# Performance work log

Hardware: AMD Instinct MI355X
Metric: run time of the kernel (lower is better)

The kernel has to match this reference:

```python
import jax, jax.numpy as jnp
import numpy as np

INP_SIZE = 3072
HID = 1024
OUT = 768
N_RES = 2  # same block (shared weights) applied twice, as in the torch code
EPS = 1e-5


def _layernorm(x, g, b):
    m = jnp.mean(x, axis=-1, keepdims=True)
    v = jnp.mean((x - m) ** 2, axis=-1, keepdims=True)
    return (x - m) / jnp.sqrt(v + EPS) * g + b


def setup_inputs() -> dict:
    key = jax.random.key(0)
    ks = jax.random.split(key, 8)
    bsz = 8192
    s = 0.02
    return {
        "inp": jax.random.normal(ks[0], (bsz, INP_SIZE), dtype=jnp.float32),
        "y": jax.random.normal(ks[1], (bsz, OUT), dtype=jnp.float32),
        "ln1_g": jnp.ones((INP_SIZE,), jnp.float32),
        "ln1_b": jnp.zeros((INP_SIZE,), jnp.float32),
        "W1": jax.random.normal(ks[2], (INP_SIZE, HID), dtype=jnp.float32) * s,
        "b1": jnp.zeros((HID,), jnp.float32),
        "Wa": jax.random.normal(ks[3], (HID, HID), dtype=jnp.float32) * s,
        "ba": jnp.zeros((HID,), jnp.float32),
        "Wb": jax.random.normal(ks[4], (HID, HID), dtype=jnp.float32) * s,
        "bb": jnp.zeros((HID,), jnp.float32),
        "W2": jax.random.normal(ks[5], (HID, OUT), dtype=jnp.float32) * s,
        "b2": jnp.zeros((OUT,), jnp.float32),
        "ln2_g": jnp.ones((OUT,), jnp.float32),
        "ln2_b": jnp.zeros((OUT,), jnp.float32),
    }


def reference(inp, y, ln1_g, ln1_b, W1, b1, Wa, ba, Wb, bb, W2, b2, ln2_g, ln2_b):
    bsz = inp.shape[0]
    # backbone (dropout in eval mode = identity)
    h = _layernorm(inp, ln1_g, ln1_b) @ W1 + b1  # [bsz, HID]
    for _ in range(N_RES):  # shared block weights, applied twice
        r = jax.nn.relu(jax.nn.relu(h @ Wa + ba) @ Wb + bb)
        h = h + r
    pred_y = _layernorm(h @ W2 + b2, ln2_g, ln2_b)  # [bsz, OUT]

    # batched contrastive cosine-sim loss (replaces per-sample python loop)
    pn = pred_y / jnp.linalg.norm(pred_y, axis=1, keepdims=True)
    yn = y / jnp.linalg.norm(y, axis=1, keepdims=True)
    S = pn @ yn.T  # [bsz, bsz] cosine similarities
    loss = -jnp.sum(pn * yn) + jnp.sum(jax.nn.logsumexp(S, axis=1))

    acc = jnp.mean((jnp.argmax(S, axis=1) == jnp.arange(bsz)).astype(jnp.float32))
    return pred_y, loss, acc
```

## Files before the change

### kernel.cpp

```cpp
#include <hip/hip_runtime.h>
#include <hip/hip_fp16.h>
#include <cstdint>
#include <math.h>

#define INP  3072
#define HID  1024
#define OUTD 768
#define BSZ  8192

typedef _Float16 f16;
typedef _Float16 f16x8 __attribute__((ext_vector_type(8)));
typedef float    f32x4 __attribute__((ext_vector_type(4)));

static constexpr float LOG2E = 1.44269504088896340736f;
static constexpr float LN2   = 0.69314718055994530942f;

static constexpr size_t OFF_XH   = 0;
static constexpr size_t OFF_PN   = 0;
static constexpr size_t OFF_YN   = OFF_PN   + (size_t)BSZ*OUTD*2;
static constexpr size_t OFF_PSUM = OFF_YN   + (size_t)BSZ*OUTD*2;
static constexpr size_t OFF_PMAX = OFF_PSUM + (size_t)BSZ*64*4;
static constexpr size_t OFF_HB   = OFF_XH   + (size_t)BSZ*INP*2;
static constexpr size_t OFF_TT   = OFF_HB   + (size_t)BSZ*HID*2;
static constexpr size_t OFF_H    = OFF_TT   + (size_t)BSZ*OUTD*4;
static constexpr size_t OFF_W1T  = OFF_H    + (size_t)BSZ*HID*4;
static constexpr size_t OFF_WAT  = OFF_W1T  + (size_t)INP*HID*2;
static constexpr size_t OFF_WBT  = OFF_WAT  + (size_t)HID*HID*2;
static constexpr size_t OFF_W2T  = OFF_WBT  + (size_t)HID*HID*2;
static constexpr size_t OFF_DIAG = OFF_W2T  + (size_t)HID*OUTD*2;
static constexpr size_t OFF_ACC  = OFF_DIAG + (size_t)BSZ*4;

#define GL2LDS(gp, lp) __builtin_amdgcn_global_load_lds( \
    (__attribute__((address_space(1))) void*)(uintptr_t)(gp), \
    (__attribute__((address_space(3))) void*)(unsigned)(uintptr_t)(lp), 16, 0, 0)

__device__ __forceinline__ float blk_sum256(float v, float* sm) {
  #pragma unroll
  for (int d = 1; d < 64; d <<= 1) v += __shfl_xor(v, d, 64);
  int tid = threadIdx.x;
  __syncthreads();
  if ((tid & 63) == 0) sm[tid >> 6] = v;
  __syncthreads();
  return sm[0] + sm[1] + sm[2] + sm[3];
}

__global__ __launch_bounds__(256) void ln1_kernel(const float* __restrict__ inp,
    const float* __restrict__ g, const float* __restrict__ b, f16* __restrict__ xh) {
  __shared__ float sm[4];
  const int row = blockIdx.x, tid = threadIdx.x;
  const float* x = inp + (size_t)row * INP;
  float v[12]; float s = 0.f;
  #pragma unroll
  for (int i = 0; i < 12; i++) { v[i] = x[tid + i*256]; s += v[i]; }
  const float mean = blk_sum256(s, sm) * (1.f/INP);
  float s2 = 0.f;
  #pragma unroll
  for (int i = 0; i < 12; i++) { float d = v[i]-mean; s2 += d*d; }
  const float rstd = rsqrtf(blk_sum256(s2, sm) * (1.f/INP) + 1e-5f);
  f16* o = xh + (size_t)row * INP;
  #pragma unroll
  for (int i = 0; i < 12; i++) {
    int c = tid + i*256;
    o[c] = (f16)((v[i]-mean)*rstd*g[c] + b[c]);
  }
}

__global__ __launch_bounds__(256) void transpose_cast(const float* __restrict__ W,
    f16* __restrict__ Wt, int K, int N) {
  __shared__ float t[32][33];
  const int n0 = blockIdx.x*32, k0 = blockIdx.y*32;
  const int tx = threadIdx.x & 31, ty = threadIdx.x >> 5;
  #pragma unroll
  for (int i = 0; i < 32; i += 8) t[ty+i][tx] = W[(size_t)(k0+ty+i)*N + n0+tx];
  __syncthreads();
  #pragma unroll
  for (int i = 0; i < 32; i += 8) Wt[(size_t)(n0+ty+i)*K + k0+tx] = (f16)t[tx][ty+i];
}

__global__ __launch_bounds__(256) void ln2_kernel(const float* __restrict__ pre,
    const float* __restrict__ g, const float* __restrict__ b,
    float* __restrict__ outY, f16* __restrict__ pn) {
  __shared__ float sm[4];
  const int row = blockIdx.x, tid = threadIdx.x;
  const float* x = pre + (size_t)row * OUTD;
  float v[3]; float s = 0.f;
  #pragma unroll
  for (int i = 0; i < 3; i++) { v[i] = x[tid + i*256]; s += v[i]; }
  const float mean = blk_sum256(s, sm) * (1.f/OUTD);
  float s2 = 0.f;
  #pragma unroll
  for (int i = 0; i < 3; i++) { float d = v[i]-mean; s2 += d*d; }
  const float rstd = rsqrtf(blk_sum256(s2, sm) * (1.f/OUTD) + 1e-5f);
  float z[3]; float n2 = 0.f;
  #pragma unroll
  for (int i = 0; i < 3; i++) { int c = tid + i*256; z[i] = (v[i]-mean)*rstd*g[c] + b[c]; n2 += z[i]*z[i]; }
  const float rn = rsqrtf(blk_sum256(n2, sm)) * LOG2E;
  float* oy = outY + (size_t)row * OUTD;
  f16*   op = pn   + (size_t)row * OUTD;
  #pragma unroll
  for (int i = 0; i < 3; i++) { int c = tid + i*256; oy[c] = z[i]; op[c] = (f16)(z[i]*rn); }
}

__global__ __launch_bounds__(256) void yn_kernel(const float* __restrict__ y, f16* __restrict__ yn) {
  __shared__ float sm[4];
  const int row = blockIdx.x, tid = threadIdx.x;
  const float* x = y + (size_t)row * OUTD;
  float v[3]; float n2 = 0.f;
  #pragma unroll
  for (int i = 0; i < 3; i++) { v[i] = x[tid + i*256]; n2 += v[i]*v[i]; }
  const float rn = rsqrtf(blk_sum256(n2, sm));
  f16* o = yn + (size_t)row * OUTD;
  #pragma unroll
  for (int i = 0; i < 3; i++) { int c = tid + i*256; o[c] = (f16)(v[i]*rn); }
}

#define EPI_H   0
#define EPI_T   1
#define EPI_RES 2
#define EPI_P   3
#define EPI_S   4

template<int EPI>
__global__ __launch_bounds__(256) void gemm_bt(
    const f16* __restrict__ A, const f16* __restrict__ B, int K, int N,
    const float* __restrict__ bias, float* __restrict__ Cf, f16* __restrict__ Ch,
    const float* __restrict__ Hin,
    float* __restrict__ partsum, float* __restrict__ partmax, float* __restrict__ diagv)
{
  __shared__ alignas(16) f16 lA[2][128*32];
  __shared__ alignas(16) f16 lB[2][128*32];
  const int tid  = threadIdx.x;
  const int wave = tid >> 6, lane = tid & 63;
  const int m0 = blockIdx.x * 128, n0 = blockIdx.y * 128;
  const int srow  = tid >> 2;
  const int skc   = tid & 3;
  const int skc_sw = skc ^ ((srow >> 1) & 3);
  const f16* gA = A + (size_t)(m0 + srow) * K + skc_sw*8;
  const f16* gB = B + (size_t)(n0 + srow) * K + skc_sw*8;
  const int wm = wave & 1, wn = wave >> 1;
  const int fm = lane & 15;
  const int g4 = lane >> 4;
  const int ks = (fm >> 1) & 3;
  const int ck = ((g4 ^ ks) * 8);

  f32x4 acc[4][4];
  #pragma unroll
  for (int i = 0; i < 4; i++)
    #pragma unroll
    for (int j = 0; j < 4; j++) acc[i][j] = (f32x4){0.f,0.f,0.f,0.f};

  const int iters = K >> 5;
  auto stage = [&](int buf, int k0) {
    f16* lAw = &lA[buf][wave*16*32];
    f16* lBw = &lB[buf][wave*16*32];
    GL2LDS(gA + k0,                lAw);
    GL2LDS(gA + (size_t)64*K + k0, lAw + 64*32);
    GL2LDS(gB + k0,                lBw);
    GL2LDS(gB + (size_t)64*K + k0, lBw + 64*32);
  };

  stage(0, 0);
  __syncthreads();
  for (int it = 0; it < iters; ++it) {
    const int cur = it & 1;
    if (it + 1 < iters) stage(cur ^ 1, (it + 1) << 5);
    f16x8 af[4], bf[4];
    #pragma unroll
    for (int i = 0; i < 4; i++) af[i] = *(const f16x8*)&lA[cur][(wm*64 + i*16 + fm)*32 + ck];
    #pragma unroll
    for (int j = 0; j < 4; j++) bf[j] = *(const f16x8*)&lB[cur][(wn*64 + j*16 + fm)*32 + ck];
    #pragma unroll
    for (int i = 0; i < 4; i++)
      #pragma unroll
      for (int j = 0; j < 4; j++)
        acc[i][j] = __builtin_amdgcn_mfma_f32_16x16x32_f16(af[i], bf[j], acc[i][j], 0, 0, 0);
    __syncthreads();
  }

  if constexpr (EPI != EPI_S) {
    const int colb = n0 + wn*64;
    const int rowb = m0 + wm*64;
    #pragma unroll
    for (int i = 0; i < 4; i++) {
      #pragma unroll
      for (int j = 0; j < 4; j++) {
        const int col = colb + j*16 + fm;
        const float bs = bias[col];
        #pragma unroll
        for (int r = 0; r < 4; r++) {
          const int row = rowb + i*16 + g4*4 + r;
          float v = acc[i][j][r] + bs;
          const size_t idx = (size_t)row * N + col;
          if constexpr (EPI == EPI_H)        { Cf[idx] = v; Ch[idx] = (f16)v; }
          else if constexpr (EPI == EPI_T)   { v = fmaxf(v, 0.f); Ch[idx] = (f16)v; }
          else if constexpr (EPI == EPI_RES) { v = fmaxf(v, 0.f); v += Hin[idx]; Cf[idx] = v; Ch[idx] = (f16)v; }
          else                               { Cf[idx] = v; }
        }
      }
    }
  } else {
    __shared__ float redS[2][128], redM[2][128];
    const int bn = blockIdx.y;
    if (m0 == n0) {
      #pragma unroll
      for (int i = 0; i < 4; i++)
        #pragma unroll
        for (int j = 0; j < 4; j++) {
          const int col = n0 + wn*64 + j*16 + fm;
          #pragma unroll
          for (int r = 0; r < 4; r++) {
            const int row = m0 + wm*64 + i*16 + g4*4 + r;
            if (row == col) diagv[row] = acc[i][j][r];
          }
        }
    }
    #pragma unroll
    for (int i = 0; i < 4; i++) {
      #pragma unroll
      for (int r = 0; r < 4; r++) {
        const float a0 = acc[i][0][r], a1 = acc[i][1][r];
        const float a2 = acc[i][2][r], a3 = acc[i][3][r];
        float s  = exp2f(a0) + exp2f(a1) + exp2f(a2) + exp2f(a3);
        float mx = fmaxf(fmaxf(a0, a1), fmaxf(a2, a3));
        #pragma unroll
        for (int d = 1; d < 16; d <<= 1) {
          s  += __shfl_xor(s, d, 64);
          mx  = fmaxf(mx, __shfl_xor(mx, d, 64));
        }
        if (fm == 0) { const int lrow = wm*64 + i*16 + g4*4 + r; redS[wn][lrow] = s; redM[wn][lrow] = mx; }
      }
    }
    __syncthreads();
    if (tid < 128) {
      const float sa = redS[0][tid] + redS[1][tid];
      const float ma = fmaxf(redM[0][tid], redM[1][tid]);
      const size_t p = (size_t)bn * BSZ + m0 + tid;
      partsum[p] = sa; partmax[p] = ma;
    }
  }
}

__global__ __launch_bounds__(256) void reduce_rows(const float* __restrict__ partsum,
    const float* __restrict__ partmax, const float* __restrict__ diagv,
    float* __restrict__ accum) {
  __shared__ float sm[4];
  const int row = blockIdx.x*256 + threadIdx.x;
  float s = 0.f, mx = -1e30f;
  for (int i = 0; i < 64; i++) {
    s  += partsum[(size_t)i*BSZ + row];
    mx  = fmaxf(mx, partmax[(size_t)i*BSZ + row]);
  }
  const float dgs  = diagv[row];
  const float corr = (dgs >= mx) ? 1.f : 0.f;
  const float lse  = logf(s);
  const float dg   = dgs * LN2;
  const float lse_s = blk_sum256(lse, sm);
  const float dg_s  = blk_sum256(dg, sm);
  const float c_s   = blk_sum256(corr, sm);
  if (threadIdx.x == 0) {
    atomicAdd(&accum[0], lse_s);
    atomicAdd(&accum[1], dg_s);
    atomicAdd(&accum[2], c_s);
  }
}

__global__ void finalize_kernel(const float* __restrict__ accum, float* __restrict__ out) {
  out[0] = accum[0] - accum[1];
  out[1] = accum[2] * (1.f / BSZ);
}

extern "C" void kernel_launch(void* const* d_in, const int* in_sizes, int n_in,
                              void* d_out, int out_size, void* d_ws, size_t ws_size,
                              hipStream_t stream) {
  const float* inp  = (const float*)d_in[0];
  const float* y    = (const float*)d_in[1];
  const float* ln1g = (const float*)d_in[2];
  const float* ln1b = (const float*)d_in[3];
  const float* W1   = (const float*)d_in[4];
  const float* b1   = (const float*)d_in[5];
  const float* Wa   = (const float*)d_in[6];
  const float* ba   = (const float*)d_in[7];
  const float* Wb   = (const float*)d_in[8];
  const float* bb   = (const float*)d_in[9];
  const float* W2   = (const float*)d_in[10];
  const float* b2   = (const float*)d_in[11];
  const float* ln2g = (const float*)d_in[12];
  const float* ln2b = (const float*)d_in[13];
  float* out = (float*)d_out;

  char* ws = (char*)d_ws;
  f16*   XH   = (f16*)  (ws + OFF_XH);
  f16*   PN   = (f16*)  (ws + OFF_PN);
  f16*   YN   = (f16*)  (ws + OFF_YN);
  float* PSUM = (float*)(ws + OFF_PSUM);
  float* PMAX = (float*)(ws + OFF_PMAX);
  f16*   HB   = (f16*)  (ws + OFF_HB);
  f16*   T    = (f16*)  (ws + OFF_TT);
  float* PRE2 = (float*)(ws + OFF_TT);
  float* H    = (float*)(ws + OFF_H);
  f16*   W1T  = (f16*)  (ws + OFF_W1T);
  f16*   WAT  = (f16*)  (ws + OFF_WAT);
  f16*   WBT  = (f16*)  (ws + OFF_WBT);
  f16*   W2T  = (f16*)  (ws + OFF_W2T);
  float* DIAG = (float*)(ws + OFF_DIAG);
  float* ACC  = (float*)(ws + OFF_ACC);

  transpose_cast<<<dim3(HID/32,  INP/32), 256, 0, stream>>>(W1, W1T, INP, HID);
  transpose_cast<<<dim3(HID/32,  HID/32), 256, 0, stream>>>(Wa, WAT, HID, HID);
  transpose_cast<<<dim3(HID/32,  HID/32), 256, 0, stream>>>(Wb, WBT, HID, HID);
  transpose_cast<<<dim3(OUTD/32, HID/32), 256, 0, stream>>>(W2, W2T, HID, OUTD);

  ln1_kernel<<<BSZ, 256, 0, stream>>>(inp, ln1g, ln1b, XH);

  gemm_bt<EPI_H><<<dim3(BSZ/128, HID/128), 256, 0, stream>>>(
      XH, W1T, INP, HID, b1, H, HB, nullptr, nullptr, nullptr, nullptr);

  for (int it = 0; it < 2; it++) {
    gemm_bt<EPI_T><<<dim3(BSZ/128, HID/128), 256, 0, stream>>>(
        HB, WAT, HID, HID, ba, nullptr, T, nullptr, nullptr, nullptr, nullptr);
    gemm_bt<EPI_RES><<<dim3(BSZ/128, HID/128), 256, 0, stream>>>(
        T, WBT, HID, HID, bb, H, HB, H, nullptr, nullptr, nullptr);
  }

  gemm_bt<EPI_P><<<dim3(BSZ/128, OUTD/128), 256, 0, stream>>>(
      HB, W2T, HID, OUTD, b2, PRE2, nullptr, nullptr, nullptr, nullptr, nullptr);

  ln2_kernel<<<BSZ, 256, 0, stream>>>(PRE2, ln2g, ln2b, out, PN);
  yn_kernel<<<BSZ, 256, 0, stream>>>(y, YN);

  hipMemsetAsync(ACC, 0, 4*sizeof(float), stream);

  gemm_bt<EPI_S><<<dim3(BSZ/128, BSZ/128), 256, 0, stream>>>(
      PN, YN, OUTD, BSZ, nullptr, nullptr, nullptr, nullptr, PSUM, PMAX, DIAG);

  reduce_rows<<<BSZ/256, 256, 0, stream>>>(PSUM, PMAX, DIAG, ACC);
  finalize_kernel<<<1, 1, 0, stream>>>(ACC, out + (size_t)BSZ*OUTD);
}
```

Before: 588.7 us.

## Quantize similarity GEMM to int8, drop fp32 residual stream, fuse small kernels

The 8192x8192 cosine-similarity GEMM now runs on int8 MFMA, with normalized vectors quantized at scale 384 and rescaled in the epilogue. This halves operand bytes and doubles MFMA throughput relative to fp16. The fp32 residual copy H is removed, so the residual is carried only in fp16, which cuts global writes and reads. Separately, the four weight transposes become one launch, ln2 and yn become one launch, finalize is folded into reduce_rows via a last-block atomic counter, and ln1 is vectorized. The trade-off is precision: int8 similarities and an fp16-only residual may shift the loss and accuracy enough to fail tolerance.

```diff
diff --git a/kernel.cpp b/kernel.cpp
--- a/kernel.cpp
+++ b/kernel.cpp
@@ -10,20 +10,24 @@
 
 typedef _Float16 f16;
 typedef _Float16 f16x8 __attribute__((ext_vector_type(8)));
+typedef _Float16 f16x4 __attribute__((ext_vector_type(4)));
 typedef float    f32x4 __attribute__((ext_vector_type(4)));
+typedef int      i32x4 __attribute__((ext_vector_type(4)));
+typedef signed char s8;
 
 static constexpr float LOG2E = 1.44269504088896340736f;
 static constexpr float LN2   = 0.69314718055994530942f;
+static constexpr float QS    = 384.0f;
+static constexpr float CSC   = LOG2E / (QS * QS);
 
 static constexpr size_t OFF_XH   = 0;
 static constexpr size_t OFF_PN   = 0;
-static constexpr size_t OFF_YN   = OFF_PN   + (size_t)BSZ*OUTD*2;
-static constexpr size_t OFF_PSUM = OFF_YN   + (size_t)BSZ*OUTD*2;
+static constexpr size_t OFF_YN   = OFF_PN   + (size_t)BSZ*OUTD;
+static constexpr size_t OFF_PSUM = OFF_YN   + (size_t)BSZ*OUTD;
 static constexpr size_t OFF_PMAX = OFF_PSUM + (size_t)BSZ*64*4;
 static constexpr size_t OFF_HB   = OFF_XH   + (size_t)BSZ*INP*2;
 static constexpr size_t OFF_TT   = OFF_HB   + (size_t)BSZ*HID*2;
-static constexpr size_t OFF_H    = OFF_TT   + (size_t)BSZ*OUTD*4;
-static constexpr size_t OFF_W1T  = OFF_H    + (size_t)BSZ*HID*4;
+static constexpr size_t OFF_W1T  = OFF_TT   + (size_t)BSZ*OUTD*4;
 static constexpr size_t OFF_WAT  = OFF_W1T  + (size_t)INP*HID*2;
 static constexpr size_t OFF_WBT  = OFF_WAT  + (size_t)HID*HID*2;
 static constexpr size_t OFF_W2T  = OFF_WBT  + (size_t)HID*HID*2;
@@ -44,31 +48,56 @@
   return sm[0] + sm[1] + sm[2] + sm[3];
 }
 
+__device__ __forceinline__ s8 q8(float v) {
+  int q = __float2int_rn(v * QS);
+  q = q > 127 ? 127 : (q < -127 ? -127 : q);
+  return (s8)q;
+}
+
 __global__ __launch_bounds__(256) void ln1_kernel(const float* __restrict__ inp,
     const float* __restrict__ g, const float* __restrict__ b, f16* __restrict__ xh) {
   __shared__ float sm[4];
   const int row = blockIdx.x, tid = threadIdx.x;
-  const float* x = inp + (size_t)row * INP;
-  float v[12]; float s = 0.f;
-  #pragma unroll
-  for (int i = 0; i < 12; i++) { v[i] = x[tid + i*256]; s += v[i]; }
+  const float4* x4 = (const float4*)(inp + (size_t)row * INP);
+  float4 v[3]; float s = 0.f;
+  #pragma unroll
+  for (int i = 0; i < 3; i++) { v[i] = x4[tid + i*256]; s += v[i].x+v[i].y+v[i].z+v[i].w; }
   const float mean = blk_sum256(s, sm) * (1.f/INP);
   float s2 = 0.f;
   #pragma unroll
-  for (int i = 0; i < 12; i++) { float d = v[i]-mean; s2 += d*d; }
+  for (int i = 0; i < 3; i++) {
+    float dx=v[i].x-mean, dy=v[i].y-mean, dz=v[i].z-mean, dw=v[i].w-mean;
+    s2 += dx*dx+dy*dy+dz*dz+dw*dw;
+  }
   const float rstd = rsqrtf(blk_sum256(s2, sm) * (1.f/INP) + 1e-5f);
-  f16* o = xh + (size_t)row * INP;
-  #pragma unroll
-  for (int i = 0; i < 12; i++) {
-    int c = tid + i*256;
-    o[c] = (f16)((v[i]-mean)*rstd*g[c] + b[c]);
-  }
-}
-
-__global__ __launch_bounds__(256) void transpose_cast(const float* __restrict__ W,
-    f16* __restrict__ Wt, int K, int N) {
+  const float4* g4p = (const float4*)g;
+  const float4* b4p = (const float4*)b;
+  f16x4* o4 = (f16x4*)(xh + (size_t)row * INP);
+  #pragma unroll
+  for (int i = 0; i < 3; i++) {
+    const int c = tid + i*256;
+    const float4 gg = g4p[c], bb = b4p[c];
+    f16x4 t;
+    t[0] = (f16)((v[i].x-mean)*rstd*gg.x + bb.x);
+    t[1] = (f16)((v[i].y-mean)*rstd*gg.y + bb.y);
+    t[2] = (f16)((v[i].z-mean)*rstd*gg.z + bb.z);
+    t[3] = (f16)((v[i].w-mean)*rstd*gg.w + bb.w);
+    o4[c] = t;
+  }
+}
+
+__global__ __launch_bounds__(256) void transpose_all(
+    const float* __restrict__ W1, const float* __restrict__ Wa,
+    const float* __restrict__ Wb, const float* __restrict__ W2,
+    f16* __restrict__ W1T, f16* __restrict__ WAT,
+    f16* __restrict__ WBT, f16* __restrict__ W2T) {
   __shared__ float t[32][33];
-  const int n0 = blockIdx.x*32, k0 = blockIdx.y*32;
+  const int bI = blockIdx.x;
+  const float* W; f16* Wt; int K, N, n0, k0;
+  if (bI < 3072)      { int tt = bI;      W = W1; Wt = W1T; K = INP; N = HID;  n0 = (tt & 31)*32; k0 = (tt >> 5)*32; }
+  else if (bI < 4096) { int tt = bI-3072; W = Wa; Wt = WAT; K = HID; N = HID;  n0 = (tt & 31)*32; k0 = (tt >> 5)*32; }
+  else if (bI < 5120) { int tt = bI-4096; W = Wb; Wt = WBT; K = HID; N = HID;  n0 = (tt & 31)*32; k0 = (tt >> 5)*32; }
+  else                { int tt = bI-5120; W = W2; Wt = W2T; K = HID; N = OUTD; int kq = tt/24; n0 = (tt - kq*24)*32; k0 = kq*32; }
   const int tx = threadIdx.x & 31, ty = threadIdx.x >> 5;
   #pragma unroll
   for (int i = 0; i < 32; i += 8) t[ty+i][tx] = W[(size_t)(k0+ty+i)*N + n0+tx];
@@ -77,55 +106,54 @@
   for (int i = 0; i < 32; i += 8) Wt[(size_t)(n0+ty+i)*K + k0+tx] = (f16)t[tx][ty+i];
 }
 
-__global__ __launch_bounds__(256) void ln2_kernel(const float* __restrict__ pre,
+__global__ __launch_bounds__(256) void ln2_yn(const float* __restrict__ pre,
     const float* __restrict__ g, const float* __restrict__ b,
-    float* __restrict__ outY, f16* __restrict__ pn) {
+    const float* __restrict__ y,
+    float* __restrict__ outY, s8* __restrict__ pn, s8* __restrict__ yn) {
   __shared__ float sm[4];
-  const int row = blockIdx.x, tid = threadIdx.x;
-  const float* x = pre + (size_t)row * OUTD;
-  float v[3]; float s = 0.f;
-  #pragma unroll
-  for (int i = 0; i < 3; i++) { v[i] = x[tid + i*256]; s += v[i]; }
-  const float mean = blk_sum256(s, sm) * (1.f/OUTD);
-  float s2 = 0.f;
-  #pragma unroll
-  for (int i = 0; i < 3; i++) { float d = v[i]-mean; s2 += d*d; }
-  const float rstd = rsqrtf(blk_sum256(s2, sm) * (1.f/OUTD) + 1e-5f);
-  float z[3]; float n2 = 0.f;
-  #pragma unroll
-  for (int i = 0; i < 3; i++) { int c = tid + i*256; z[i] = (v[i]-mean)*rstd*g[c] + b[c]; n2 += z[i]*z[i]; }
-  const float rn = rsqrtf(blk_sum256(n2, sm)) * LOG2E;
-  float* oy = outY + (size_t)row * OUTD;
-  f16*   op = pn   + (size_t)row * OUTD;
-  #pragma unroll
-  for (int i = 0; i < 3; i++) { int c = tid + i*256; oy[c] = z[i]; op[c] = (f16)(z[i]*rn); }
-}
-
-__global__ __launch_bounds__(256) void yn_kernel(const float* __restrict__ y, f16* __restrict__ yn) {
-  __shared__ float sm[4];
-  const int row = blockIdx.x, tid = threadIdx.x;
-  const float* x = y + (size_t)row * OUTD;
-  float v[3]; float n2 = 0.f;
-  #pragma unroll
-  for (int i = 0; i < 3; i++) { v[i] = x[tid + i*256]; n2 += v[i]*v[i]; }
-  const float rn = rsqrtf(blk_sum256(n2, sm));
-  f16* o = yn + (size_t)row * OUTD;
-  #pragma unroll
-  for (int i = 0; i < 3; i++) { int c = tid + i*256; o[c] = (f16)(v[i]*rn); }
+  const int tid = threadIdx.x;
+  if ((int)blockIdx.x < BSZ) {
+    const int row = blockIdx.x;
+    const float* x = pre + (size_t)row * OUTD;
+    float v[3]; float s = 0.f;
+    #pragma unroll
+    for (int i = 0; i < 3; i++) { v[i] = x[tid + i*256]; s += v[i]; }
+    const float mean = blk_sum256(s, sm) * (1.f/OUTD);
+    float s2 = 0.f;
+    #pragma unroll
+    for (int i = 0; i < 3; i++) { float d = v[i]-mean; s2 += d*d; }
+    const float rstd = rsqrtf(blk_sum256(s2, sm) * (1.f/OUTD) + 1e-5f);
+    float z[3]; float n2 = 0.f;
+    #pragma unroll
+    for (int i = 0; i < 3; i++) { int c = tid + i*256; z[i] = (v[i]-mean)*rstd*g[c] + b[c]; n2 += z[i]*z[i]; }
+    const float rn = rsqrtf(blk_sum256(n2, sm));
+    float* oy = outY + (size_t)row * OUTD;
+    s8*   op = pn   + (size_t)row * OUTD;
+    #pragma unroll
+    for (int i = 0; i < 3; i++) { int c = tid + i*256; oy[c] = z[i]; op[c] = q8(z[i]*rn); }
+  } else {
+    const int row = blockIdx.x - BSZ;
+    const float* x = y + (size_t)row * OUTD;
+    float v[3]; float n2 = 0.f;
+    #pragma unroll
+    for (int i = 0; i < 3; i++) { v[i] = x[tid + i*256]; n2 += v[i]*v[i]; }
+    const float rn = rsqrtf(blk_sum256(n2, sm));
+    s8* o = yn + (size_t)row * OUTD;
+    #pragma unroll
+    for (int i = 0; i < 3; i++) { int c = tid + i*256; o[c] = q8(v[i]*rn); }
+  }
 }
 
 #define EPI_H   0
 #define EPI_T   1
 #define EPI_RES 2
 #define EPI_P   3
-#define EPI_S   4
 
 template<int EPI>
 __global__ __launch_bounds__(256) void gemm_bt(
     const f16* __restrict__ A, const f16* __restrict__ B, int K, int N,
     const float* __restrict__ bias, float* __restrict__ Cf, f16* __restrict__ Ch,
-    const float* __restrict__ Hin,
-    float* __restrict__ partsum, float* __restrict__ partmax, float* __restrict__ diagv)
+    const f16* __restrict__ Hin)
 {
   __shared__ alignas(16) f16 lA[2][128*32];
   __shared__ alignas(16) f16 lB[2][128*32];
@@ -177,72 +205,127 @@
     __syncthreads();
   }
 
-  if constexpr (EPI != EPI_S) {
-    const int colb = n0 + wn*64;
-    const int rowb = m0 + wm*64;
-    #pragma unroll
-    for (int i = 0; i < 4; i++) {
+  const int colb = n0 + wn*64;
+  const int rowb = m0 + wm*64;
+  #pragma unroll
+  for (int i = 0; i < 4; i++) {
+    #pragma unroll
+    for (int j = 0; j < 4; j++) {
+      const int col = colb + j*16 + fm;
+      const float bs = bias[col];
+      #pragma unroll
+      for (int r = 0; r < 4; r++) {
+        const int row = rowb + i*16 + g4*4 + r;
+        float v = acc[i][j][r] + bs;
+        const size_t idx = (size_t)row * N + col;
+        if constexpr (EPI == EPI_H)        { Ch[idx] = (f16)v; }
+        else if constexpr (EPI == EPI_T)   { v = fmaxf(v, 0.f); Ch[idx] = (f16)v; }
+        else if constexpr (EPI == EPI_RES) { v = fmaxf(v, 0.f); v += (float)Hin[idx]; Ch[idx] = (f16)v; }
+        else                               { Cf[idx] = v; }
+      }
+    }
+  }
+}
+
+__global__ __launch_bounds__(256) void gemm_s8(
+    const s8* __restrict__ A, const s8* __restrict__ B,
+    float* __restrict__ partsum, float* __restrict__ partmax, float* __restrict__ diagv)
+{
+  __shared__ alignas(16) s8 lA[2][128*64];
+  __shared__ alignas(16) s8 lB[2][128*64];
+  __shared__ float redS[2][128], redM[2][128];
+  const int K = OUTD;
+  const int tid = threadIdx.x;
+  const int wave = tid >> 6, lane = tid & 63;
+  const int m0 = blockIdx.x * 128, n0 = blockIdx.y * 128;
+  const int srow = tid >> 2;
+  const int cl   = tid & 3;
+  const int cg   = cl ^ ((srow ^ (srow >> 2)) & 3);
+  const s8* gA = A + (size_t)(m0 + srow) * K + cg*16;
+  const s8* gB = B + (size_t)(n0 + srow) * K + cg*16;
+  const int wm = wave & 1, wn = wave >> 1;
+  const int fm = lane & 15;
+  const int g4 = lane >> 4;
+  const int ksw = (fm ^ (fm >> 2)) & 3;
+  const int ck8 = (g4 ^ ksw) * 16;
+
+  i32x4 acc[4][4];
+  #pragma unroll
+  for (int i = 0; i < 4; i++)
+    #pragma unroll
+    for (int j = 0; j < 4; j++) acc[i][j] = (i32x4){0,0,0,0};
+
+  auto stage = [&](int buf, int k0) {
+    s8* lAw = &lA[buf][wave*16*64];
+    s8* lBw = &lB[buf][wave*16*64];
+    GL2LDS(gA + k0,                lAw);
+    GL2LDS(gA + (size_t)64*K + k0, lAw + 64*64);
+    GL2LDS(gB + k0,                lBw);
+    GL2LDS(gB + (size_t)64*K + k0, lBw + 64*64);
+  };
+
+  stage(0, 0);
+  __syncthreads();
+  const int iters = K / 64;
+  for (int it = 0; it < iters; ++it) {
+    const int cur = it & 1;
+    if (it + 1 < iters) stage(cur ^ 1, (it + 1) * 64);
+    i32x4 af[4], bf[4];
+    #pragma unroll
+    for (int i = 0; i < 4; i++) af[i] = *(const i32x4*)&lA[cur][(wm*64 + i*16 + fm)*64 + ck8];
+    #pragma unroll
+    for (int j = 0; j < 4; j++) bf[j] = *(const i32x4*)&lB[cur][(wn*64 + j*16 + fm)*64 + ck8];
+    #pragma unroll
+    for (int i = 0; i < 4; i++)
+      #pragma unroll
+      for (int j = 0; j < 4; j++)
+        acc[i][j] = __builtin_amdgcn_mfma_i32_16x16x64_i8(af[i], bf[j], acc[i][j], 0, 0, 0);
+    __syncthreads();
+  }
+
+  if (m0 == n0) {
+    #pragma unroll
+    for (int i = 0; i < 4; i++)
       #pragma unroll
       for (int j = 0; j < 4; j++) {
-        const int col = colb + j*16 + fm;
-        const float bs = bias[col];
+        const int col = n0 + wn*64 + j*16 + fm;
         #pragma unroll
         for (int r = 0; r < 4; r++) {
-          const int row = rowb + i*16 + g4*4 + r;
-          float v = acc[i][j][r] + bs;
-          const size_t idx = (size_t)row * N + col;
-          if constexpr (EPI == EPI_H)        { Cf[idx] = v; Ch[idx] = (f16)v; }
-          else if constexpr (EPI == EPI_T)   { v = fmaxf(v, 0.f); Ch[idx] = (f16)v; }
-          else if constexpr (EPI == EPI_RES) { v = fmaxf(v, 0.f); v += Hin[idx]; Cf[idx] = v; Ch[idx] = (f16)v; }
-          else                               { Cf[idx] = v; }
+          const int row = m0 + wm*64 + i*16 + g4*4 + r;
+          if (row == col) diagv[row] = (float)acc[i][j][r] * CSC;
         }
       }
+  }
+  #pragma unroll
+  for (int i = 0; i < 4; i++) {
+    #pragma unroll
+    for (int r = 0; r < 4; r++) {
+      const float a0 = (float)acc[i][0][r] * CSC;
+      const float a1 = (float)acc[i][1][r] * CSC;
+      const float a2 = (float)acc[i][2][r] * CSC;
+      const float a3 = (float)acc[i][3][r] * CSC;
+      float s  = exp2f(a0) + exp2f(a1) + exp2f(a2) + exp2f(a3);
+      float mx = fmaxf(fmaxf(a0, a1), fmaxf(a2, a3));
+      #pragma unroll
+      for (int d = 1; d < 16; d <<= 1) {
+        s  += __shfl_xor(s, d, 64);
+        mx  = fmaxf(mx, __shfl_xor(mx, d, 64));
+      }
+      if (fm == 0) { const int lrow = wm*64 + i*16 + g4*4 + r; redS[wn][lrow] = s; redM[wn][lrow] = mx; }
     }
-  } else {
-    __shared__ float redS[2][128], redM[2][128];
-    const int bn = blockIdx.y;
-    if (m0 == n0) {
-      #pragma unroll
-      for (int i = 0; i < 4; i++)
-        #pragma unroll
-        for (int j = 0; j < 4; j++) {
-          const int col = n0 + wn*64 + j*16 + fm;
-          #pragma unroll
-          for (int r = 0; r < 4; r++) {
-            const int row = m0 + wm*64 + i*16 + g4*4 + r;
-            if (row == col) diagv[row] = acc[i][j][r];
-          }
-        }
-    }
-    #pragma unroll
-    for (int i = 0; i < 4; i++) {
-      #pragma unroll
-      for (int r = 0; r < 4; r++) {
-        const float a0 = acc[i][0][r], a1 = acc[i][1][r];
-        const float a2 = acc[i][2][r], a3 = acc[i][3][r];
-        float s  = exp2f(a0) + exp2f(a1) + exp2f(a2) + exp2f(a3);
-        float mx = fmaxf(fmaxf(a0, a1), fmaxf(a2, a3));
-        #pragma unroll
-        for (int d = 1; d < 16; d <<= 1) {
-          s  += __shfl_xor(s, d, 64);
-          mx  = fmaxf(mx, __shfl_xor(mx, d, 64));
-        }
-        if (fm == 0) { const int lrow = wm*64 + i*16 + g4*4 + r; redS[wn][lrow] = s; redM[wn][lrow] = mx; }
-      }
-    }
-    __syncthreads();
-    if (tid < 128) {
-      const float sa = redS[0][tid] + redS[1][tid];
-      const float ma = fmaxf(redM[0][tid], redM[1][tid]);
-      const size_t p = (size_t)bn * BSZ + m0 + tid;
-      partsum[p] = sa; partmax[p] = ma;
-    }
+  }
+  __syncthreads();
+  if (tid < 128) {
+    const float sa = redS[0][tid] + redS[1][tid];
+    const float ma = fmaxf(redM[0][tid], redM[1][tid]);
+    const size_t p = (size_t)blockIdx.y * BSZ + m0 + tid;
+    partsum[p] = sa; partmax[p] = ma;
   }
 }
 
 __global__ __launch_bounds__(256) void reduce_rows(const float* __restrict__ partsum,
     const float* __restrict__ partmax, const float* __restrict__ diagv,
-    float* __restrict__ accum) {
+    float* __restrict__ accum, float* __restrict__ out) {
   __shared__ float sm[4];
   const int row = blockIdx.x*256 + threadIdx.x;
   float s = 0.f, mx = -1e30f;
@@ -261,12 +344,16 @@
     atomicAdd(&accum[0], lse_s);
     atomicAdd(&accum[1], dg_s);
     atomicAdd(&accum[2], c_s);
-  }
-}
-
-__global__ void finalize_kernel(const float* __restrict__ accum, float* __restrict__ out) {
-  out[0] = accum[0] - accum[1];
-  out[1] = accum[2] * (1.f / BSZ);
+    __threadfence();
+    const unsigned old = atomicAdd((unsigned*)&accum[3], 1u);
+    if (old == gridDim.x - 1) {
+      const float a0 = atomicAdd(&accum[0], 0.f);
+      const float a1 = atomicAdd(&accum[1], 0.f);
+      const float a2 = atomicAdd(&accum[2], 0.f);
+      out[0] = a0 - a1;
+      out[1] = a2 * (1.f / BSZ);
+    }
+  }
 }
 
 extern "C" void kernel_launch(void* const* d_in, const int* in_sizes, int n_in,
@@ -290,14 +377,13 @@
 
   char* ws = (char*)d_ws;
   f16*   XH   = (f16*)  (ws + OFF_XH);
-  f16*   PN   = (f16*)  (ws + OFF_PN);
-  f16*   YN   = (f16*)  (ws + OFF_YN);
+  s8*    PN   = (s8*)   (ws + OFF_PN);
+  s8*    YN   = (s8*)   (ws + OFF_YN);
   float* PSUM = (float*)(ws + OFF_PSUM);
   float* PMAX = (float*)(ws + OFF_PMAX);
   f16*   HB   = (f16*)  (ws + OFF_HB);
   f16*   T    = (f16*)  (ws + OFF_TT);
   float* PRE2 = (float*)(ws + OFF_TT);
-  float* H    = (float*)(ws + OFF_H);
   f16*   W1T  = (f16*)  (ws + OFF_W1T);
   f16*   WAT  = (f16*)  (ws + OFF_WAT);
   f16*   WBT  = (f16*)  (ws + OFF_WBT);
@@ -305,34 +391,27 @@
   float* DIAG = (float*)(ws + OFF_DIAG);
   float* ACC  = (float*)(ws + OFF_ACC);
 
-  transpose_cast<<<dim3(HID/32,  INP/32), 256, 0, stream>>>(W1, W1T, INP, HID);
-  transpose_cast<<<dim3(HID/32,  HID/32), 256, 0, stream>>>(Wa, WAT, HID, HID);
-  transpose_cast<<<dim3(HID/32,  HID/32), 256, 0, stream>>>(Wb, WBT, HID, HID);
-  transpose_cast<<<dim3(OUTD/32, HID/32), 256, 0, stream>>>(W2, W2T, HID, OUTD);
-
+  transpose_all<<<5888, 256, 0, stream>>>(W1, Wa, Wb, W2, W1T, WAT, WBT, W2T);
   ln1_kernel<<<BSZ, 256, 0, stream>>>(inp, ln1g, ln1b, XH);
 
   gemm_bt<EPI_H><<<dim3(BSZ/128, HID/128), 256, 0, stream>>>(
-      XH, W1T, INP, HID, b1, H, HB, nullptr, nullptr, nullptr, nullptr);
+      XH, W1T, INP, HID, b1, nullptr, HB, nullptr);
 
   for (int it = 0; it < 2; it++) {
     gemm_bt<EPI_T><<<dim3(BSZ/128, HID/128), 256, 0, stream>>>(
-        HB, WAT, HID, HID, ba, nullptr, T, nullptr, nullptr, nullptr, nullptr);
+        HB, WAT, HID, HID, ba, nullptr, T, nullptr);
     gemm_bt<EPI_RES><<<dim3(BSZ/128, HID/128), 256, 0, stream>>>(
-        T, WBT, HID, HID, bb, H, HB, H, nullptr, nullptr, nullptr);
+        T, WBT, HID, HID, bb, nullptr, HB, HB);
   }
 
   gemm_bt<EPI_P><<<dim3(BSZ/128, OUTD/128), 256, 0, stream>>>(
-      HB, W2T, HID, OUTD, b2, PRE2, nullptr, nullptr, nullptr, nullptr, nullptr);
-
-  ln2_kernel<<<BSZ, 256, 0, stream>>>(PRE2, ln2g, ln2b, out, PN);
-  yn_kernel<<<BSZ, 256, 0, stream>>>(y, YN);
+      HB, W2T, HID, OUTD, b2, PRE2, nullptr, nullptr);
+
+  ln2_yn<<<2*BSZ, 256, 0, stream>>>(PRE2, ln2g, ln2b, y, out, PN, YN);
 
   hipMemsetAsync(ACC, 0, 4*sizeof(float), stream);
 
-  gemm_bt<EPI_S><<<dim3(BSZ/128, BSZ/128), 256, 0, stream>>>(
-      PN, YN, OUTD, BSZ, nullptr, nullptr, nullptr, nullptr, PSUM, PMAX, DIAG);
-
-  reduce_rows<<<BSZ/256, 256, 0, stream>>>(PSUM, PMAX, DIAG, ACC);
-  finalize_kernel<<<1, 1, 0, stream>>>(ACC, out + (size_t)BSZ*OUTD);
-}
+  gemm_s8<<<dim3(BSZ/128, BSZ/128), 256, 0, stream>>>(PN, YN, PSUM, PMAX, DIAG);
+
+  reduce_rows<<<BSZ/256, 256, 0, stream>>>(PSUM, PMAX, DIAG, ACC, out + (size_t)BSZ*OUTD);
+}
```

Measured after the change: 497.0 us. 15.6% less time.
